# Kernel optimization log

Measured on AMD Instinct MI355X. Metric: run time of the kernel, lower is better.

Reference implementation:

```python
import jax, jax.numpy as jnp
import numpy as np

EMA = 0.99
THRESH = 0.8
EPS = 1e-8


def setup_inputs() -> dict:
    key = jax.random.key(0)
    k1, k2, k3, k4 = jax.random.split(key, 4)
    B, C, M = 8192, 2048, 8192
    return {
        "features": jax.random.normal(k1, (B, C), dtype=jnp.float32),
        "confidence": jax.random.uniform(k2, (B,), dtype=jnp.float32),
        "mem_features": jax.random.normal(k3, (M, C), dtype=jnp.float32),
        "mem_confidences": jax.random.uniform(k4, (M,), dtype=jnp.float32),
        "ptr0": 4096,
        "filled0": 4096,
    }


def _update(mem_feat, mem_conf, ptr0, filled0, features, confidence):
    M = mem_feat.shape[0]

    def step(carry, xs):
        mf, mc, ptr, filled = carry
        feat, conf = xs
        is_high = conf > THRESH
        p = jnp.mod(ptr, M)
        exists = filled > p
        cur_f = mf[p]          # [C]
        cur_c = mc[p]
        upd_f = jnp.where(exists, EMA * cur_f + (1.0 - EMA) * feat, feat)
        upd_c = jnp.where(exists, EMA * cur_c + (1.0 - EMA) * conf, conf)
        new_f = jnp.where(is_high, upd_f, cur_f)
        new_c = jnp.where(is_high, upd_c, cur_c)
        mf = mf.at[p].set(new_f)
        mc = mc.at[p].set(new_c)
        filled = filled + jnp.where(is_high & (~exists), 1, 0).astype(filled.dtype)
        ptr = ptr + jnp.where(is_high, 1, 0).astype(ptr.dtype)
        return (mf, mc, ptr, filled), None

    init = (mem_feat, mem_conf,
            jnp.asarray(ptr0, jnp.int32), jnp.asarray(filled0, jnp.int32))
    (mf, mc, ptr, filled), _ = jax.lax.scan(step, init, (features, confidence))
    return mf, mc, filled


def reference(features, confidence, mem_features, mem_confidences, ptr0, filled0):
    mf, mc, filled = _update(mem_features, mem_confidences, ptr0, filled0,
                             features, confidence)
    M, C = mf.shape
    # confidence-weighted stats over valid slots [:filled] (mask, jit-safe)
    valid = (jnp.arange(M) < filled).astype(mf.dtype)
    w = mc * valid                              # [M]
    total = jnp.sum(w) + EPS
    mean = jnp.einsum("mc,m->c", mf, w) / total  # [C]
    diff = mf - mean[None, :]
    var = jnp.einsum("mc,m->c", diff * diff, w) / total
    std = jnp.sqrt(var + EPS)
    # pack: updated memory bank + weighted mean + weighted std -> [M+2, C]
    return jnp.concatenate([mf, mean[None, :], std[None, :]], axis=0)
```

## Files before the change

kernel.cpp:

```cpp
#include <hip/hip_runtime.h>
#include <math.h>

#define EMA_A 0.99f
#define EMA_B 0.01f
#define THRESH 0.8f
#define EPS_F 1e-8f

#define NBLK2 256
#define RPB   32


__global__ __launch_bounds__(1024)
void k_scan(const float* __restrict__ conf,
            const float* __restrict__ mem_conf,
            const int* __restrict__ ptr0_p,
            const int* __restrict__ filled0_p,
            int* __restrict__ hdr,
            int* __restrict__ slot_info,
            float* __restrict__ w,
            int B, int M)
{
    const int tid  = threadIdx.x;
    const int lane = tid & 63;
    const int wave = tid >> 6;

    for (int m = tid; m < M; m += 1024) slot_info[m] = -1;

    const int base_i = tid * 8;
    int mask = 0;
    #pragma unroll
    for (int k = 0; k < 8; ++k) {
        int i = base_i + k;
        float c = (i < B) ? conf[i] : 0.0f;
        mask |= (c > THRESH) ? (1 << k) : 0;
    }
    int cnt = __popc(mask);

    __shared__ int s_cnt[1024];
    __shared__ int s_gbase[64];
    __shared__ int s_scalars[2];
    s_cnt[tid] = cnt;
    __syncthreads();

    if (tid < 64) {
        int sum16 = 0;
        #pragma unroll
        for (int u = 0; u < 16; ++u) sum16 += s_cnt[tid * 16 + u];
        int v = sum16;
        #pragma unroll
        for (int d = 1; d < 64; d <<= 1) {
            int o = __shfl_up(v, d, 64);
            if (lane >= d) v += o;
        }
        s_gbase[tid] = v - sum16;
        if (tid == 63) s_scalars[0] = v;
    }
    __syncthreads();
    const int K = s_scalars[0];

    int j = s_gbase[tid >> 4];
    for (int u = (tid & ~15); u < tid; ++u) j += s_cnt[u];

    int P0 = ((ptr0_p[0] % M) + M) % M;
    int F0 = filled0_p[0];
    if (F0 < 0) F0 = 0;
    if (F0 > M) F0 = M;
    const int L0 = M - P0;
    const int F1 = F0 + (M - (P0 > F0 ? P0 : F0));

    #pragma unroll
    for (int k = 0; k < 8; ++k) {
        if (mask & (1 << k)) {
            int exist;
            if (j < L0)          exist = (P0 + j) < F0 ? 1 : 0;
            else if (j < L0 + M) exist = (j - L0) < F1 ? 1 : 0;
            else                 exist = 1;
            int p = (P0 + j) % M;
            slot_info[p] = ((base_i + k) << 1) | exist;
            ++j;
        }
    }

    if (tid == 0) {
        int n0 = K < L0 ? K : L0;
        int e0 = F0 - P0; if (e0 < 0) e0 = 0; if (e0 > n0) e0 = n0;
        int fresh0 = n0 - e0;
        int n1 = K - L0; if (n1 < 0) n1 = 0; if (n1 > M) n1 = M;
        int fresh1 = n1 - F1; if (fresh1 < 0) fresh1 = 0;
        int filled = F0 + fresh0 + fresh1;
        if (filled > M) filled = M;
        s_scalars[1] = filled;
        hdr[0] = K;
        hdr[1] = filled;
    }
    __syncthreads();
    const int filled = s_scalars[1];

    float acc = 0.0f;
    for (int m = tid; m < M; m += 1024) {
        int info = slot_info[m];
        float mco = mem_conf[m];
        float mcu;
        if (info >= 0) {
            float c = conf[info >> 1];
            mcu = (info & 1) ? (EMA_A * mco + EMA_B * c) : c;
        } else {
            mcu = mco;
        }
        float wm = (m < filled) ? mcu : 0.0f;
        w[m] = wm;
        acc += wm;
    }
    #pragma unroll
    for (int d = 32; d >= 1; d >>= 1) acc += __shfl_down(acc, d, 64);
    __shared__ float s_red[16];
    if (lane == 0) s_red[wave] = acc;
    __syncthreads();
    if (tid == 0) {
        float s = 0.0f;
        for (int u = 0; u < 16; ++u) s += s_red[u];
        ((float*)hdr)[2] = s;
    }
}


__device__ __forceinline__ float4 f4_ema(float4 m, float4 f) {
    float4 r;
    r.x = EMA_A * m.x + EMA_B * f.x;
    r.y = EMA_A * m.y + EMA_B * f.y;
    r.z = EMA_A * m.z + EMA_B * f.z;
    r.w = EMA_A * m.w + EMA_B * f.w;
    return r;
}

__global__ __launch_bounds__(512)
void k_update(const float* __restrict__ mem_feat,
              const float* __restrict__ feat,
              const int* __restrict__ slot_info,
              const float* __restrict__ w,
              float* __restrict__ out,
              float* __restrict__ p1,
              float* __restrict__ p2,
              int C)
{
    const int blk = blockIdx.x, tid = threadIdx.x;
    const int c0 = tid * 4;

    __shared__ int   s_info[RPB];
    __shared__ float s_w[RPB];
    const int row0 = blk * RPB;
    if (tid < RPB) {
        s_info[tid] = slot_info[row0 + tid];
        s_w[tid]    = w[row0 + tid];
    }
    __syncthreads();

    float4 s1 = {0.f, 0.f, 0.f, 0.f};
    float4 s2 = {0.f, 0.f, 0.f, 0.f};

    #pragma unroll 4
    for (int r = 0; r < RPB; ++r) {
        const int m = row0 + r;
        const size_t base = (size_t)m * C;
        float4 mv = *(const float4*)(mem_feat + base + c0);
        const int info = s_info[r];
        float4 x;
        if (info >= 0) {
            float4 fv = *(const float4*)(feat + (size_t)(info >> 1) * C + c0);
            x = (info & 1) ? f4_ema(mv, fv) : fv;
        } else {
            x = mv;
        }
        const float wv = s_w[r];
        s1.x += wv * x.x; s1.y += wv * x.y; s1.z += wv * x.z; s1.w += wv * x.w;
        s2.x += wv * x.x * x.x; s2.y += wv * x.y * x.y;
        s2.z += wv * x.z * x.z; s2.w += wv * x.w * x.w;
        *(float4*)(out + base + c0) = x;
    }
    const size_t pb = (size_t)blk * C;
    *(float4*)(p1 + pb + c0) = s1;
    *(float4*)(p2 + pb + c0) = s2;
}


__global__ __launch_bounds__(256)
void k_stats(const float* __restrict__ p1,
             const float* __restrict__ p2,
             const float* __restrict__ hdrf,
             float* __restrict__ out,
             int M, int C)
{
    const int cc = threadIdx.x & 31;
    const int chunk = threadIdx.x >> 5;
    const int c = blockIdx.x * 32 + cc;
    double s1 = 0.0, s2 = 0.0;
    for (int bb = 0; bb < 32; ++bb) {
        int b = chunk * 32 + bb;
        s1 += (double)p1[(size_t)b * C + c];
        s2 += (double)p2[(size_t)b * C + c];
    }
    __shared__ double l1[256], l2[256];
    l1[threadIdx.x] = s1;
    l2[threadIdx.x] = s2;
    __syncthreads();
    if (chunk == 0) {
        for (int q = 1; q < 8; ++q) { s1 += l1[cc + 32 * q]; s2 += l2[cc + 32 * q]; }
        double sumw  = (double)hdrf[2];
        double total = sumw + (double)EPS_F;
        double mean  = s1 / total;
        double var   = (s2 - 2.0 * mean * s1 + mean * mean * sumw) / total;
        out[(size_t)M * C + c]       = (float)mean;
        out[(size_t)(M + 1) * C + c] = (float)sqrt(var + (double)EPS_F);
    }
}


extern "C" void kernel_launch(void* const* d_in, const int* in_sizes, int n_in,
                              void* d_out, int out_size, void* d_ws, size_t ws_size,
                              hipStream_t stream)
{
    const float* features     = (const float*)d_in[0];
    const float* confidence   = (const float*)d_in[1];
    const float* mem_features = (const float*)d_in[2];
    const float* mem_conf     = (const float*)d_in[3];
    const int*   ptr0         = (const int*)d_in[4];
    const int*   filled0      = (const int*)d_in[5];

    const int B = in_sizes[1];
    const int M = in_sizes[3];
    const int C = in_sizes[0] / B;

    char* ws = (char*)d_ws;
    int*   hdr       = (int*)ws;
    int*   slot_info = (int*)(ws + 1024);
    float* w         = (float*)(ws + 1024 + 4 * (size_t)M);
    float* p1        = (float*)(ws + 1024 + 8 * (size_t)M);
    float* p2        = (float*)(ws + 1024 + 8 * (size_t)M + 4 * (size_t)NBLK2 * C);

    float* out = (float*)d_out;

    k_scan<<<1, 1024, 0, stream>>>(confidence, mem_conf, ptr0, filled0,
                                   hdr, slot_info, w, B, M);
    k_update<<<NBLK2, 512, 0, stream>>>(mem_features, features, slot_info, w,
                                        out, p1, p2, C);
    k_stats<<<C / 32, 256, 0, stream>>>(p1, p2, (const float*)hdr, out, M, C);
}
```

Measured before the change: 196.6 us.

## Move weight computation into update kernel, double grid, skip unneeded row loads

The single-block scan kernel no longer computes per-slot weights and their sum. Each update block now derives its own weights from slot_info, confidences and the filled count, and writes a per-block weight partial that the stats kernel reduces. The update grid doubles to 512 blocks of 16 rows, only the rows actually needed are loaded per branch, and output stores are nontemporal. This shortens the serial single-block phase and raises parallelism, at the cost of twice as many partial-sum rows for the stats kernel to reduce.

```diff
diff --git a/kernel.cpp b/kernel.cpp
--- a/kernel.cpp
+++ b/kernel.cpp
@@ -6,23 +6,22 @@
 #define THRESH 0.8f
 #define EPS_F 1e-8f
 
-#define NBLK2 256
-#define RPB   32
+#define NBLK2 512
+#define RPB   16
+
+typedef float fx4 __attribute__((ext_vector_type(4)));
 
 
 __global__ __launch_bounds__(1024)
 void k_scan(const float* __restrict__ conf,
-            const float* __restrict__ mem_conf,
             const int* __restrict__ ptr0_p,
             const int* __restrict__ filled0_p,
             int* __restrict__ hdr,
             int* __restrict__ slot_info,
-            float* __restrict__ w,
             int B, int M)
 {
     const int tid  = threadIdx.x;
     const int lane = tid & 63;
-    const int wave = tid >> 6;
 
     for (int m = tid; m < M; m += 1024) slot_info[m] = -1;
 
@@ -38,7 +37,6 @@
 
     __shared__ int s_cnt[1024];
     __shared__ int s_gbase[64];
-    __shared__ int s_scalars[2];
     s_cnt[tid] = cnt;
     __syncthreads();
 
@@ -53,10 +51,10 @@
             if (lane >= d) v += o;
         }
         s_gbase[tid] = v - sum16;
-        if (tid == 63) s_scalars[0] = v;
-    }
-    __syncthreads();
-    const int K = s_scalars[0];
+        if (tid == 63) hdr[0] = v;
+    }
+    __syncthreads();
+    const int K = hdr[0];
 
     int j = s_gbase[tid >> 4];
     for (int u = (tid & ~15); u < tid; ++u) j += s_cnt[u];
@@ -89,56 +87,20 @@
         int fresh1 = n1 - F1; if (fresh1 < 0) fresh1 = 0;
         int filled = F0 + fresh0 + fresh1;
         if (filled > M) filled = M;
-        s_scalars[1] = filled;
-        hdr[0] = K;
         hdr[1] = filled;
     }
-    __syncthreads();
-    const int filled = s_scalars[1];
-
-    float acc = 0.0f;
-    for (int m = tid; m < M; m += 1024) {
-        int info = slot_info[m];
-        float mco = mem_conf[m];
-        float mcu;
-        if (info >= 0) {
-            float c = conf[info >> 1];
-            mcu = (info & 1) ? (EMA_A * mco + EMA_B * c) : c;
-        } else {
-            mcu = mco;
-        }
-        float wm = (m < filled) ? mcu : 0.0f;
-        w[m] = wm;
-        acc += wm;
-    }
-    #pragma unroll
-    for (int d = 32; d >= 1; d >>= 1) acc += __shfl_down(acc, d, 64);
-    __shared__ float s_red[16];
-    if (lane == 0) s_red[wave] = acc;
-    __syncthreads();
-    if (tid == 0) {
-        float s = 0.0f;
-        for (int u = 0; u < 16; ++u) s += s_red[u];
-        ((float*)hdr)[2] = s;
-    }
-}
-
-
-__device__ __forceinline__ float4 f4_ema(float4 m, float4 f) {
-    float4 r;
-    r.x = EMA_A * m.x + EMA_B * f.x;
-    r.y = EMA_A * m.y + EMA_B * f.y;
-    r.z = EMA_A * m.z + EMA_B * f.z;
-    r.w = EMA_A * m.w + EMA_B * f.w;
-    return r;
-}
+}
+
 
 __global__ __launch_bounds__(512)
 void k_update(const float* __restrict__ mem_feat,
               const float* __restrict__ feat,
+              const float* __restrict__ conf,
+              const float* __restrict__ mem_conf,
               const int* __restrict__ slot_info,
-              const float* __restrict__ w,
+              const int* __restrict__ hdr,
               float* __restrict__ out,
+              float* __restrict__ p0,
               float* __restrict__ p1,
               float* __restrict__ p2,
               int C)
@@ -150,62 +112,88 @@
     __shared__ float s_w[RPB];
     const int row0 = blk * RPB;
     if (tid < RPB) {
-        s_info[tid] = slot_info[row0 + tid];
-        s_w[tid]    = w[row0 + tid];
-    }
-    __syncthreads();
-
-    float4 s1 = {0.f, 0.f, 0.f, 0.f};
-    float4 s2 = {0.f, 0.f, 0.f, 0.f};
+        const int m = row0 + tid;
+        const int info = slot_info[m];
+        const int filled = hdr[1];
+        const float mco = mem_conf[m];
+        float mcu = mco;
+        if (info >= 0) {
+            float c = conf[info >> 1];
+            mcu = (info & 1) ? (EMA_A * mco + EMA_B * c) : c;
+        }
+        s_info[tid] = info;
+        s_w[tid]    = (m < filled) ? mcu : 0.0f;
+    }
+    __syncthreads();
+    if (tid == 0) {
+        float s = 0.0f;
+        #pragma unroll
+        for (int r = 0; r < RPB; ++r) s += s_w[r];
+        p0[blk] = s;
+    }
+
+    fx4 s1 = {0.f, 0.f, 0.f, 0.f};
+    fx4 s2 = {0.f, 0.f, 0.f, 0.f};
 
     #pragma unroll 4
     for (int r = 0; r < RPB; ++r) {
         const int m = row0 + r;
         const size_t base = (size_t)m * C;
-        float4 mv = *(const float4*)(mem_feat + base + c0);
         const int info = s_info[r];
-        float4 x;
-        if (info >= 0) {
-            float4 fv = *(const float4*)(feat + (size_t)(info >> 1) * C + c0);
-            x = (info & 1) ? f4_ema(mv, fv) : fv;
+        fx4 x;
+        if (info < 0) {
+            x = *(const fx4*)(mem_feat + base + c0);
+        } else if (info & 1) {
+            fx4 mv = *(const fx4*)(mem_feat + base + c0);
+            fx4 fv = *(const fx4*)(feat + (size_t)(info >> 1) * C + c0);
+            x = EMA_A * mv + EMA_B * fv;
         } else {
-            x = mv;
+            x = *(const fx4*)(feat + (size_t)(info >> 1) * C + c0);
         }
         const float wv = s_w[r];
-        s1.x += wv * x.x; s1.y += wv * x.y; s1.z += wv * x.z; s1.w += wv * x.w;
-        s2.x += wv * x.x * x.x; s2.y += wv * x.y * x.y;
-        s2.z += wv * x.z * x.z; s2.w += wv * x.w * x.w;
-        *(float4*)(out + base + c0) = x;
+        s1 += wv * x;
+        s2 += wv * x * x;
+        __builtin_nontemporal_store(x, (fx4*)(out + base + c0));
     }
     const size_t pb = (size_t)blk * C;
-    *(float4*)(p1 + pb + c0) = s1;
-    *(float4*)(p2 + pb + c0) = s2;
+    *(fx4*)(p1 + pb + c0) = s1;
+    *(fx4*)(p2 + pb + c0) = s2;
 }
 
 
 __global__ __launch_bounds__(256)
-void k_stats(const float* __restrict__ p1,
+void k_stats(const float* __restrict__ p0,
+             const float* __restrict__ p1,
              const float* __restrict__ p2,
-             const float* __restrict__ hdrf,
              float* __restrict__ out,
              int M, int C)
 {
-    const int cc = threadIdx.x & 31;
-    const int chunk = threadIdx.x >> 5;
+    const int tid = threadIdx.x;
+
+    __shared__ float s_sw[4];
+    float sw = 0.0f;
+    for (int i = tid; i < NBLK2; i += 256) sw += p0[i];
+    #pragma unroll
+    for (int d = 32; d >= 1; d >>= 1) sw += __shfl_down(sw, d, 64);
+    if ((tid & 63) == 0) s_sw[tid >> 6] = sw;
+    __syncthreads();
+
+    const int cc = tid & 31;
+    const int chunk = tid >> 5;
     const int c = blockIdx.x * 32 + cc;
     double s1 = 0.0, s2 = 0.0;
-    for (int bb = 0; bb < 32; ++bb) {
-        int b = chunk * 32 + bb;
+    for (int bb = 0; bb < NBLK2 / 8; ++bb) {
+        int b = chunk * (NBLK2 / 8) + bb;
         s1 += (double)p1[(size_t)b * C + c];
         s2 += (double)p2[(size_t)b * C + c];
     }
     __shared__ double l1[256], l2[256];
-    l1[threadIdx.x] = s1;
-    l2[threadIdx.x] = s2;
+    l1[tid] = s1;
+    l2[tid] = s2;
     __syncthreads();
     if (chunk == 0) {
         for (int q = 1; q < 8; ++q) { s1 += l1[cc + 32 * q]; s2 += l2[cc + 32 * q]; }
-        double sumw  = (double)hdrf[2];
+        double sumw  = (double)(s_sw[0] + s_sw[1] + s_sw[2] + s_sw[3]);
         double total = sumw + (double)EPS_F;
         double mean  = s1 / total;
         double var   = (s2 - 2.0 * mean * s1 + mean * mean * sumw) / total;
@@ -233,15 +221,14 @@
     char* ws = (char*)d_ws;
     int*   hdr       = (int*)ws;
     int*   slot_info = (int*)(ws + 1024);
-    float* w         = (float*)(ws + 1024 + 4 * (size_t)M);
-    float* p1        = (float*)(ws + 1024 + 8 * (size_t)M);
-    float* p2        = (float*)(ws + 1024 + 8 * (size_t)M + 4 * (size_t)NBLK2 * C);
+    float* p0        = (float*)(ws + 1024 + 4 * (size_t)M);
+    float* p1        = (float*)(ws + 65536);
+    float* p2        = (float*)(ws + 65536 + 4 * (size_t)NBLK2 * C);
 
     float* out = (float*)d_out;
 
-    k_scan<<<1, 1024, 0, stream>>>(confidence, mem_conf, ptr0, filled0,
-                                   hdr, slot_info, w, B, M);
-    k_update<<<NBLK2, 512, 0, stream>>>(mem_features, features, slot_info, w,
-                                        out, p1, p2, C);
-    k_stats<<<C / 32, 256, 0, stream>>>(p1, p2, (const float*)hdr, out, M, C);
-}
+    k_scan<<<1, 1024, 0, stream>>>(confidence, ptr0, filled0, hdr, slot_info, B, M);
+    k_update<<<NBLK2, 512, 0, stream>>>(mem_features, features, confidence, mem_conf,
+                                        slot_info, hdr, out, p0, p1, p2, C);
+    k_stats<<<C / 32, 256, 0, stream>>>(p0, p1, p2, out, M, C);
+}
```

Result: faster. 185.6 us (-5.6%).
